# Performance work log

Hardware: AMD Instinct MI355X
Metric: run time of the kernel (lower is better)

Reference implementation:

```python
import jax, jax.numpy as jnp
import numpy as np

NEG_SLOPE = 0.2  # PyG GATConv default leaky_relu slope
NUM_GRAPHS = 64


def gat_layer(x, src, dst, W, a_src, a_dst, b, heads, out_ch, concat, N):
    # x: [N, in_ch] -> h: [N, H, C]
    h = (x @ W).reshape(N, heads, out_ch)
    a_s = jnp.einsum('nhc,hc->nh', h, a_src)  # [N, H]
    a_d = jnp.einsum('nhc,hc->nh', h, a_dst)  # [N, H]
    e = jax.nn.leaky_relu(a_s[src] + a_d[dst], NEG_SLOPE)  # [E, H]
    # segment softmax over edges grouped by destination node
    emax = jax.ops.segment_max(e, dst, num_segments=N)
    emax = jnp.where(jnp.isfinite(emax), emax, 0.0)
    ex = jnp.exp(e - emax[dst])
    denom = jax.ops.segment_sum(ex, dst, num_segments=N)
    alpha = ex / (denom[dst] + 1e-16)  # [E, H]
    out = jax.ops.segment_sum(alpha[:, :, None] * h[src], dst, num_segments=N)  # [N, H, C]
    out = out.reshape(N, heads * out_ch) if concat else out.mean(axis=1)
    return out + b


def setup_inputs() -> dict:
    key = jax.random.key(0)
    ks = jax.random.split(key, 16)
    N, E, F_IN, H, C, NC = 50000, 800000, 128, 4, 64, 200
    x = jax.random.normal(ks[0], (N, F_IN), dtype=jnp.float32)
    edge_index = jax.random.randint(ks[1], (2, E), 0, N, dtype=jnp.int32)
    batch = jnp.sort(jax.random.randint(ks[2], (N,), 0, NUM_GRAPHS, dtype=jnp.int32))
    s = 0.05
    params = dict(
        W1=jax.random.normal(ks[3], (F_IN, H * C), jnp.float32) * s,
        a_src1=jax.random.normal(ks[4], (H, C), jnp.float32) * s,
        a_dst1=jax.random.normal(ks[5], (H, C), jnp.float32) * s,
        b1=jnp.zeros((H * C,), jnp.float32),
        W2=jax.random.normal(ks[6], (H * C, H * C), jnp.float32) * s,
        a_src2=jax.random.normal(ks[7], (H, C), jnp.float32) * s,
        a_dst2=jax.random.normal(ks[8], (H, C), jnp.float32) * s,
        b2=jnp.zeros((H * C,), jnp.float32),
        W3=jax.random.normal(ks[9], (H * C, C), jnp.float32) * s,
        a_src3=jax.random.normal(ks[10], (1, C), jnp.float32) * s,
        a_dst3=jax.random.normal(ks[11], (1, C), jnp.float32) * s,
        b3=jnp.zeros((C,), jnp.float32),
        Wc=jax.random.normal(ks[12], (C, NC), jnp.float32) * s,
        bc=jnp.zeros((NC,), jnp.float32),
    )
    return dict(x=x, edge_index=edge_index, batch=batch, **params)


def reference(x, edge_index, batch,
              W1, a_src1, a_dst1, b1,
              W2, a_src2, a_dst2, b2,
              W3, a_src3, a_dst3, b3,
              Wc, bc):
    N = x.shape[0]
    # PyG GATConv adds self-loops by default
    loop = jnp.arange(N, dtype=edge_index.dtype)
    src = jnp.concatenate([edge_index[0], loop])
    dst = jnp.concatenate([edge_index[1], loop])
    H, C = a_src1.shape
    h = gat_layer(x, src, dst, W1, a_src1, a_dst1, b1, H, C, True, N)
    h = jax.nn.elu(h)  # dropout is identity in eval mode
    h = gat_layer(h, src, dst, W2, a_src2, a_dst2, b2, H, C, True, N)
    h = jax.nn.elu(h)
    h = gat_layer(h, src, dst, W3, a_src3, a_dst3, b3, 1, C, False, N)
    h = jax.nn.elu(h)
    # global mean pool per graph
    sums = jax.ops.segment_sum(h, batch, num_segments=NUM_GRAPHS)
    counts = jax.ops.segment_sum(jnp.ones((N,), h.dtype), batch, num_segments=NUM_GRAPHS)
    pooled = sums / jnp.maximum(counts, 1.0)[:, None]
    return pooled @ Wc + bc
```

## Files before the change

kernel.cpp:

```cpp
#include <hip/hip_runtime.h>


typedef __attribute__((ext_vector_type(8))) __bf16 bf16x8;
typedef __attribute__((ext_vector_type(4))) float f32x4;
typedef __attribute__((ext_vector_type(8))) unsigned short u16x8;

#define LOG2E 1.44269504f

static __device__ __forceinline__ unsigned short f2bf(float f) {
    unsigned u = __float_as_uint(f);
    unsigned r = (u + 0x7fffu + ((u >> 16) & 1u)) >> 16;
    return (unsigned short)r;
}
static __device__ __forceinline__ float bf2f(unsigned short s) {
    return __uint_as_float(((unsigned)s) << 16);
}

static __device__ __forceinline__ void g2lds16(const unsigned short* g,
                                               unsigned short* l) {
    __builtin_amdgcn_global_load_lds(
        (const __attribute__((address_space(1))) unsigned int*)g,
        (__attribute__((address_space(3))) unsigned int*)l, 16, 0, 0);
}

__global__ void count_edges(const int* __restrict__ ei, int* __restrict__ deg,
                            int* __restrict__ epos, int E) {
    int i = blockIdx.x * blockDim.x + threadIdx.x;
    if (i >= E) return;
    int dst = ei[E + i];
    epos[i] = atomicAdd(&deg[dst], 1);
}

__global__ __launch_bounds__(256) void scan_partial(const int* __restrict__ deg,
                                                    int* __restrict__ rowptr,
                                                    int* __restrict__ blockSums, int N) {
    int t = threadIdx.x;
    int lane = t & 63, wv = t >> 6;
    int base = blockIdx.x * 1024 + t * 4;
    int v[4];
#pragma unroll
    for (int j = 0; j < 4; ++j) v[j] = (base + j < N) ? deg[base + j] + 1 : 0;
    int local = v[0] + v[1] + v[2] + v[3];
    int x = local;
#pragma unroll
    for (int off = 1; off < 64; off <<= 1) {
        int y = __shfl_up(x, off);
        if (lane >= off) x += y;
    }
    __shared__ int wsum[4];
    if (lane == 63) wsum[wv] = x;
    __syncthreads();
    int woff = 0;
    for (int i = 0; i < wv; ++i) woff += wsum[i];
    int run = woff + x - local;
#pragma unroll
    for (int j = 0; j < 4; ++j) {
        if (base + j < N) rowptr[base + j] = run;
        run += v[j];
    }
    if (t == 255) blockSums[blockIdx.x] = woff + x;
}

__global__ void scan_blocks(int* __restrict__ blockSums, int* __restrict__ rowptr,
                            int NB, int N) {
    int lane = threadIdx.x;
    int carry = 0;
    for (int b0 = 0; b0 < NB; b0 += 64) {
        int i = b0 + lane;
        int v = (i < NB) ? blockSums[i] : 0;
        int x = v;
#pragma unroll
        for (int off = 1; off < 64; off <<= 1) {
            int y = __shfl_up(x, off);
            if (lane >= off) x += y;
        }
        if (i < NB) blockSums[i] = carry + x - v;
        carry += __shfl(x, 63);
    }
    if (lane == 0) {
        int c = N >> 10;
        int offN;
        if (c < NB) {
            offN = blockSums[c];
        } else {
            blockSums[c] = 0;
            offN = 0;
        }
        rowptr[N] = carry - offN;
    }
}

__global__ void scatter_edges(const int* __restrict__ ei, const int* __restrict__ rowptr,
                              const int* __restrict__ bs,
                              const int* __restrict__ deg, const int* __restrict__ epos,
                              int* __restrict__ srcs, int E, int N) {
    int i = blockIdx.x * blockDim.x + threadIdx.x;
    int tot = E + N;
    if (i >= tot) return;
    if (i < E) {
        int dst = ei[E + i];
        srcs[rowptr[dst] + bs[dst >> 10] + epos[i]] = ei[i];
    } else {
        int d = i - E;
        srcs[rowptr[d] + bs[d >> 10] + deg[d]] = d;
    }
}

__global__ void prep_cast(const float* __restrict__ W1, unsigned short* __restrict__ Wt1,
                          const float* __restrict__ W2, unsigned short* __restrict__ Wt2,
                          const float* __restrict__ W3, unsigned short* __restrict__ Wt3,
                          int n1, int n2, int n3, int F_IN, int HC, int C) {
    int i = blockIdx.x * blockDim.x + threadIdx.x;
    if (i < n1) {
        int n = i / F_IN, k = i - n * F_IN;
        Wt1[i] = f2bf(W1[(size_t)k * HC + n]);
        return;
    }
    i -= n1;
    if (i < n2) {
        int n = i / HC, k = i - n * HC;
        Wt2[i] = f2bf(W2[(size_t)k * HC + n]);
        return;
    }
    i -= n2;
    if (i < n3) {
        int n = i / HC, k = i - n * HC;
        Wt3[i] = f2bf(W3[(size_t)k * C + n]);
    }
}

__global__ void prep_asd(const float* __restrict__ W1, const float* __restrict__ as1,
                         const float* __restrict__ ad1,
                         const float* __restrict__ W2, const float* __restrict__ as2,
                         const float* __restrict__ ad2,
                         const float* __restrict__ W3, const float* __restrict__ as3,
                         const float* __restrict__ ad3,
                         unsigned short* __restrict__ wasd1,
                         unsigned short* __restrict__ wasd2,
                         unsigned short* __restrict__ wasd3) {
    int i = blockIdx.x * blockDim.x + threadIdx.x;
    if (i < 16 * 128) {
        int p = i >> 7, k = i & 127;
        float v = 0.f;
        if (p < 8) {
            const float* a = (p < 4) ? as1 : ad1;
            int hh = p & 3;
            for (int c = 0; c < 64; ++c)
                v += W1[(size_t)k * 256 + hh * 64 + c] * a[hh * 64 + c];
        }
        wasd1[i] = f2bf(v);
        return;
    }
    i -= 16 * 128;
    if (i < 16 * 256) {
        int p = i >> 8, k = i & 255;
        float v = 0.f;
        if (p < 8) {
            const float* a = (p < 4) ? as2 : ad2;
            int hh = p & 3;
            for (int c = 0; c < 64; ++c)
                v += W2[(size_t)k * 256 + hh * 64 + c] * a[hh * 64 + c];
        }
        wasd2[i] = f2bf(v);
        return;
    }
    i -= 16 * 256;
    if (i < 16 * 256) {
        int p = i >> 8, k = i & 255;
        float v = 0.f;
        if (p < 2) {
            const float* a = p ? ad3 : as3;
            for (int c = 0; c < 64; ++c)
                v += W3[(size_t)k * 64 + c] * a[c];
        }
        wasd3[i] = f2bf(v);
    }
}

#define BK 32

template <bool AF32, int WAVES_N>
__global__ __launch_bounds__(256) void gemm_bf16(const void* __restrict__ Av,
                                                 const unsigned short* __restrict__ Bt,
                                                 const unsigned short* __restrict__ Wasd,
                                                 unsigned short* __restrict__ C,
                                                 float* __restrict__ as_o,
                                                 float* __restrict__ ad_o,
                                                 int M, int N, int K, int H) {
    constexpr int BMt = (4 / WAVES_N) * 64;
    constexpr int BNt = WAVES_N * 64;
    constexpr int ASLOTS = BMt * 4;
    constexpr int ROUNDS = (BMt + BNt) / 64;
    constexpr bool ASD_ALL = (WAVES_N == 1);
    __shared__ unsigned short As[2][BMt * BK];
    __shared__ unsigned short Bs[2][BNt * BK];
    __shared__ unsigned short Ws[2][16 * BK];
    int t = threadIdx.x;
    int bm = blockIdx.y * BMt;
    int wave = t >> 6, lane = t & 63;
    int wm = (wave / WAVES_N) * 64, wn = (wave % WAVES_N) * 64;
    int quad = lane >> 4, mr = lane & 15;

    f32x4 zero = {0.f, 0.f, 0.f, 0.f};
    f32x4 acc[4][4];
#pragma unroll
    for (int i = 0; i < 4; ++i)
#pragma unroll
        for (int j = 0; j < 4; ++j) acc[i][j] = zero;
    f32x4 acc4[4];
#pragma unroll
    for (int i = 0; i < 4; ++i) acc4[i] = zero;

    int sw = quad ^ ((mr >> 1) & 3);
    int aoff[4], boff[4];
#pragma unroll
    for (int i = 0; i < 4; ++i) {
        aoff[i] = (wm + i * 16 + mr) * BK + sw * 8;
        boff[i] = (wn + i * 16 + mr) * BK + sw * 8;
    }

    auto stage_ab = [&](int bsel, int kk) {
        const unsigned short* Ab = (const unsigned short*)Av;
#pragma unroll
        for (int r = 0; r < ROUNDS; ++r) {
            int slotw = r * 256 + wave * 64;
            int slot = slotw + lane;
            if (slotw < ASLOTS) {
                int row = slot >> 2;
                int sg = (slot & 3) ^ ((row >> 1) & 3);
                int gra = bm + row;
                if (gra < M)
                    g2lds16(&Ab[(size_t)gra * K + kk + sg * 8], &As[bsel][slotw * 8]);
            } else {
                int bslot = slot - ASLOTS;
                int row = bslot >> 2;
                int sg = (bslot & 3) ^ ((row >> 1) & 3);
                g2lds16(&Bt[(size_t)row * K + kk + sg * 8], &Bs[bsel][(slotw - ASLOTS) * 8]);
            }
        }
        if (wave == 0)
            g2lds16(&Wasd[(size_t)(lane >> 2) * K + kk + (lane & 3) * 8], &Ws[bsel][0]);
    };
    auto stage_b_af32 = [&](int bsel, int kk) {
#pragma unroll
        for (int r = 0; r < BNt / 64; ++r) {
            int slotw = r * 256 + wave * 64;
            int bslot = slotw + lane;
            int row = bslot >> 2;
            int sg = (bslot & 3) ^ ((row >> 1) & 3);
            g2lds16(&Bt[(size_t)row * K + kk + sg * 8], &Bs[bsel][slotw * 8]);
        }
        if (wave == 0)
            g2lds16(&Wasd[(size_t)(lane >> 2) * K + kk + (lane & 3) * 8], &Ws[bsel][0]);
    };
    auto loadA_f32 = [&](int kk, float4& lo, float4& hi) {
        int slot = t, row = slot >> 2;
        int sg = (slot & 3) ^ ((row >> 1) & 3);
        int gra = bm + row;
        lo = make_float4(0.f, 0.f, 0.f, 0.f); hi = lo;
        if (gra < M) {
            const float* Af = (const float*)Av;
            lo = *(const float4*)&Af[(size_t)gra * K + kk + sg * 8];
            hi = *(const float4*)&Af[(size_t)gra * K + kk + sg * 8 + 4];
        }
    };
    auto writeA = [&](int bsel, float4 lo, float4 hi) {
        int slot = t;
        *(ushort4*)&As[bsel][slot * 8]     = make_ushort4(f2bf(lo.x), f2bf(lo.y), f2bf(lo.z), f2bf(lo.w));
        *(ushort4*)&As[bsel][slot * 8 + 4] = make_ushort4(f2bf(hi.x), f2bf(hi.y), f2bf(hi.z), f2bf(hi.w));
    };

    const int nt = K / BK;
    int cur = 0;

    if (AF32) {
        float4 l0, h0;
        loadA_f32(0, l0, h0);
        writeA(0, l0, h0);
        stage_b_af32(0, 0);
    } else {
        stage_ab(0, 0);
    }
    __syncthreads();

    for (int ts = 0; ts < nt; ++ts) {
        int nxt = cur ^ 1;
        bool more = (ts + 1 < nt);
        float4 plo, phi;
        if (more) {
            if (AF32) {
                loadA_f32((ts + 1) * BK, plo, phi);
                stage_b_af32(nxt, (ts + 1) * BK);
            } else {
                stage_ab(nxt, (ts + 1) * BK);
            }
        }
        bf16x8 af[4], bfr[4];
#pragma unroll
        for (int i = 0; i < 4; ++i) {
            af[i]  = *(bf16x8*)&As[cur][aoff[i]];
            bfr[i] = *(bf16x8*)&Bs[cur][boff[i]];
        }
#pragma unroll
        for (int i = 0; i < 4; ++i)
#pragma unroll
            for (int j = 0; j < 4; ++j)
                acc[i][j] = __builtin_amdgcn_mfma_f32_16x16x32_bf16(af[i], bfr[j], acc[i][j], 0, 0, 0);
        if (ASD_ALL || wave == 0) {
            bf16x8 wsf = *(bf16x8*)&Ws[cur][mr * BK + quad * 8];
#pragma unroll
            for (int i = 0; i < 4; ++i)
                acc4[i] = __builtin_amdgcn_mfma_f32_16x16x32_bf16(af[i], wsf, acc4[i], 0, 0, 0);
        }
        if (more && AF32) writeA(nxt, plo, phi);
        __syncthreads();
        cur = nxt;
    }

    if ((ASD_ALL || wave == 0) && mr < 2 * H) {
#pragma unroll
        for (int i = 0; i < 4; ++i)
#pragma unroll
            for (int r = 0; r < 4; ++r) {
                int grow = bm + wm + i * 16 + quad * 4 + r;
                if (grow >= M) continue;
                float v = acc4[i][r] * LOG2E;
                if (mr < H) as_o[(size_t)grow * H + mr] = v;
                else        ad_o[(size_t)grow * H + (mr - H)] = v;
            }
    }

#pragma unroll
    for (int i = 0; i < 4; ++i) {
#pragma unroll
        for (int r = 0; r < 4; ++r) {
            int grow = bm + wm + i * 16 + quad * 4 + r;
            if (grow >= M) continue;
#pragma unroll
            for (int j = 0; j < 4; ++j) {
                int gcol = wn + j * 16 + mr;
                C[(size_t)grow * N + gcol] = f2bf(acc[i][j][r]);
            }
        }
    }
}

template <int H, int NPW, int VPL, bool OUTF32>
__global__ __launch_bounds__(256) void gat_aggregate(const unsigned short* __restrict__ hbuf,
                                                     const float* __restrict__ as_i,
                                                     const float* __restrict__ ad_i,
                                                     const int* __restrict__ rowptr,
                                                     const int* __restrict__ bs,
                                                     const int* __restrict__ srcs,
                                                     const float* __restrict__ bias,
                                                     void* __restrict__ out_v, int N) {
    constexpr int LPN = 64 / NPW;
    constexpr int HC = LPN * VPL;
    int wid = (blockIdx.x * blockDim.x + threadIdx.x) >> 6;
    int lane = threadIdx.x & 63;
    int sub = lane / LPN;
    int li  = lane % LPN;
    int node = wid * NPW + sub;
    if (node >= N) return;
    int row = rowptr[node] + bs[node >> 10];
    int end = rowptr[node + 1] + bs[(node + 1) >> 10];
    int len = end - row;
    const int hd_lane = (li * VPL) >> 6;

    float advh = ad_i[(size_t)node * H + hd_lane];

    float acc[VPL];
#pragma unroll
    for (int j = 0; j < VPL; ++j) acc[j] = 0.f;
    float l = 0.f;

    const int U = 8;
    for (int base = 0; base < len; base += U) {
        int s[U];
        float cf[U];
#pragma unroll
        for (int u = 0; u < U; ++u) {
            int idx = base + u;
            int ii = row + ((idx < len) ? idx : (len - 1));
            s[u] = srcs[ii];
        }
#pragma unroll
        for (int u = 0; u < U; ++u) cf[u] = as_i[(size_t)s[u] * H + hd_lane];
        if (VPL == 8) {
            u16x8 r[U];
#pragma unroll
            for (int u = 0; u < U; ++u)
                r[u] = *(const u16x8*)&hbuf[(size_t)s[u] * HC + li * 8];
#pragma unroll
            for (int u = 0; u < U; ++u) {
                float e = cf[u] + advh;
                e = fmaxf(e, 0.2f * e);
                float wgt = (base + u < len) ? exp2f(e) : 0.f;
                l += wgt;
#pragma unroll
                for (int j = 0; j < 8; ++j) acc[j] += wgt * bf2f(r[u][j]);
            }
        } else {
            ushort4 r[U];
#pragma unroll
            for (int u = 0; u < U; ++u)
                r[u] = *(const ushort4*)&hbuf[(size_t)s[u] * HC + li * 4];
#pragma unroll
            for (int u = 0; u < U; ++u) {
                float e = cf[u] + advh;
                e = fmaxf(e, 0.2f * e);
                float wgt = (base + u < len) ? exp2f(e) : 0.f;
                l += wgt;
                acc[0] += wgt * bf2f(r[u].x);
                acc[1] += wgt * bf2f(r[u].y);
                acc[2] += wgt * bf2f(r[u].z);
                acc[3] += wgt * bf2f(r[u].w);
            }
        }
    }

    float inv_l = 1.f / (l + 1e-16f);
    float vals[VPL];
#pragma unroll
    for (int j = 0; j < VPL; ++j) {
        float v = acc[j] * inv_l + bias[li * VPL + j];
        vals[j] = (v > 0.f) ? v : (__expf(v) - 1.f);
    }
    if (OUTF32) {
        float* out = (float*)out_v;
        if (VPL == 4) {
            float4 o = make_float4(vals[0], vals[1], vals[2], vals[3]);
            *(float4*)&out[(size_t)node * HC + li * 4] = o;
        } else {
#pragma unroll
            for (int j = 0; j < VPL; ++j)
                out[(size_t)node * HC + li * VPL + j] = vals[j];
        }
    } else {
        unsigned short* out = (unsigned short*)out_v;
        if (VPL == 8) {
            u16x8 o;
#pragma unroll
            for (int j = 0; j < 8; ++j) o[j] = f2bf(vals[j]);
            *(u16x8*)&out[(size_t)node * HC + li * 8] = o;
        } else {
            ushort4 o;
            o.x = f2bf(vals[0]); o.y = f2bf(vals[1]);
            o.z = f2bf(vals[2]); o.w = f2bf(vals[3]);
            *(ushort4*)&out[(size_t)node * HC + li * 4] = o;
        }
    }
}

#define POOL_CHUNK 128
__global__ __launch_bounds__(256) void pool_kernel(const float* __restrict__ hf,
                                                   const int* __restrict__ batch,
                                                   float* __restrict__ sums,
                                                   float* __restrict__ counts, int N) {
    int t = threadIdx.x;
    int c = t & 63, sub = t >> 6;
    int start = blockIdx.x * POOL_CHUNK;
    int end = min(start + POOL_CHUNK, N);
    float acc = 0.f, cnt = 0.f;
    int cur = -1;
    for (int n = start + sub; n < end; n += 4) {
        int g = batch[n];
        if (g != cur) {
            if (cur >= 0) {
                atomicAdd(&sums[cur * 64 + c], acc);
                if (c == 0) atomicAdd(&counts[cur], cnt);
            }
            cur = g; acc = 0.f; cnt = 0.f;
        }
        acc += hf[(size_t)n * 64 + c];
        cnt += 1.f;
    }
    if (cur >= 0) {
        atomicAdd(&sums[cur * 64 + c], acc);
        if (c == 0) atomicAdd(&counts[cur], cnt);
    }
}

__global__ void classify(const float* __restrict__ sums, const float* __restrict__ counts,
                         const float* __restrict__ Wc, const float* __restrict__ bc,
                         float* __restrict__ out, int NC) {
    __shared__ float p[64];
    int g = blockIdx.x;
    if (threadIdx.x < 64) {
        float cnt = fmaxf(counts[g], 1.0f);
        p[threadIdx.x] = sums[g * 64 + threadIdx.x] / cnt;
    }
    __syncthreads();
    int k = threadIdx.x;
    if (k < NC) {
        float acc = bc[k];
        for (int c = 0; c < 64; ++c) acc += p[c] * Wc[c * NC + k];
        out[g * NC + k] = acc;
    }
}

static inline size_t align_up(size_t x, size_t a) { return (x + a - 1) / a * a; }

extern "C" void kernel_launch(void* const* d_in, const int* in_sizes, int n_in,
                              void* d_out, int out_size, void* d_ws, size_t ws_size,
                              hipStream_t stream) {
    const float* x      = (const float*)d_in[0];
    const int*   ei     = (const int*)d_in[1];
    const int*   batch  = (const int*)d_in[2];
    const float* W1     = (const float*)d_in[3];
    const float* a_src1 = (const float*)d_in[4];
    const float* a_dst1 = (const float*)d_in[5];
    const float* b1     = (const float*)d_in[6];
    const float* W2     = (const float*)d_in[7];
    const float* a_src2 = (const float*)d_in[8];
    const float* a_dst2 = (const float*)d_in[9];
    const float* b2     = (const float*)d_in[10];
    const float* W3     = (const float*)d_in[11];
    const float* a_src3 = (const float*)d_in[12];
    const float* a_dst3 = (const float*)d_in[13];
    const float* b3     = (const float*)d_in[14];
    const float* Wc     = (const float*)d_in[15];
    const float* bc     = (const float*)d_in[16];

    const int N    = in_sizes[2];
    const int E    = in_sizes[1] / 2;
    const int F_IN = in_sizes[0] / N;
    const int HC   = in_sizes[6];
    const int C    = in_sizes[14];
    const int NC   = in_sizes[16];
    const int Etot = E + N;
    const int NB   = (N + 1023) / 1024;
    const int NPB  = (N + POOL_CHUNK - 1) / POOL_CHUNK;

    char* w = (char*)d_ws;
    size_t off = 0;
    auto alloc = [&](size_t bytes) -> void* {
        void* p = w + off;
        off = align_up(off + bytes, 256);
        return p;
    };
    int*   deg    = (int*)alloc((size_t)N * 4);
    float* sums   = (float*)alloc((size_t)(64 * 64 + 64) * 4);
    float* counts = sums + 64 * 64;
    int*   rowptr = (int*)alloc((size_t)(N + 1) * 4);
    int*   epos   = (int*)alloc((size_t)E * 4);
    int*   srcs   = (int*)alloc((size_t)Etot * 4);
    int*   bsums  = (int*)alloc((size_t)(NB + 1) * 4);
    float* as_buf = (float*)alloc((size_t)N * 4 * 4);
    float* ad_buf = (float*)alloc((size_t)N * 4 * 4);
    unsigned short* Wt1 = (unsigned short*)alloc((size_t)HC * F_IN * 2);
    unsigned short* Wt2 = (unsigned short*)alloc((size_t)HC * HC * 2);
    unsigned short* Wt3 = (unsigned short*)alloc((size_t)C * HC * 2);
    unsigned short* wasd1 = (unsigned short*)alloc((size_t)16 * F_IN * 2);
    unsigned short* wasd2 = (unsigned short*)alloc((size_t)16 * HC * 2);
    unsigned short* wasd3 = (unsigned short*)alloc((size_t)16 * HC * 2);
    unsigned short* hA  = (unsigned short*)alloc((size_t)N * HC * 2);
    unsigned short* hB  = (unsigned short*)alloc((size_t)N * HC * 2);
    unsigned short* hC  = (unsigned short*)alloc((size_t)N * C * 2);
    float* bufF   = (float*)alloc((size_t)N * C * 4);

    const int TPB = 256;

    hipMemsetAsync(deg, 0, (char*)(sums + 64 * 64 + 64) - (char*)deg, stream);

    count_edges<<<(E + TPB - 1) / TPB, TPB, 0, stream>>>(ei, deg, epos, E);
    scan_partial<<<NB, 256, 0, stream>>>(deg, rowptr, bsums, N);
    scan_blocks<<<1, 64, 0, stream>>>(bsums, rowptr, NB, N);
    scatter_edges<<<(Etot + TPB - 1) / TPB, TPB, 0, stream>>>(ei, rowptr, bsums, deg, epos, srcs, E, N);

    int n1 = HC * F_IN, n2 = HC * HC, n3 = C * HC;
    int ntot = n1 + n2 + n3;
    prep_cast<<<(ntot + TPB - 1) / TPB, TPB, 0, stream>>>(
        W1, Wt1, W2, Wt2, W3, Wt3, n1, n2, n3, F_IN, HC, C);
    int nasd = 16 * F_IN + 16 * HC + 16 * HC;
    prep_asd<<<(nasd + TPB - 1) / TPB, TPB, 0, stream>>>(
        W1, a_src1, a_dst1, W2, a_src2, a_dst2, W3, a_src3, a_dst3,
        wasd1, wasd2, wasd3);

    dim3 gWide(1, (N + 63) / 64);
    dim3 gNarrow(1, (N + 255) / 256);
    int aggBlocks12 = (((N + 1) / 2) + 3) / 4;
    int aggBlocks3  = (((N + 3) / 4) + 3) / 4;

    gemm_bf16<true, 4><<<gWide, 256, 0, stream>>>(x, Wt1, wasd1, hA, as_buf, ad_buf, N, HC, F_IN, 4);
    gat_aggregate<4, 2, 8, false><<<aggBlocks12, 256, 0, stream>>>(hA, as_buf, ad_buf, rowptr, bsums, srcs, b1, hB, N);

    gemm_bf16<false, 4><<<gWide, 256, 0, stream>>>(hB, Wt2, wasd2, hA, as_buf, ad_buf, N, HC, HC, 4);
    gat_aggregate<4, 2, 8, false><<<aggBlocks12, 256, 0, stream>>>(hA, as_buf, ad_buf, rowptr, bsums, srcs, b2, hB, N);

    gemm_bf16<false, 1><<<gNarrow, 256, 0, stream>>>(hB, Wt3, wasd3, hC, as_buf, ad_buf, N, C, HC, 1);
    gat_aggregate<1, 4, 4, true><<<aggBlocks3, 256, 0, stream>>>(hC, as_buf, ad_buf, rowptr, bsums, srcs, b3, bufF, N);

    pool_kernel<<<NPB, 256, 0, stream>>>(bufF, batch, sums, counts, N);
    classify<<<64, 256, 0, stream>>>(sums, counts, Wc, bc, (float*)d_out, NC);
}
```

Before: 398.6 us.

## Merge weight prep kernels, drop GEMM double buffering, split aggregation launches

The two weight-preparation kernels become one launch. The GEMM loses its double-buffered LDS pipeline and uses single-buffered staging with two barriers per K step, halving shared memory and possibly raising occupancy, but it no longer overlaps loads with MFMA work. The layer 1 and 2 aggregations are each split into two launches over node halves. This adds launch overhead and brings no obvious benefit on a single stream.

```diff
diff --git a/kernel.cpp b/kernel.cpp
--- a/kernel.cpp
+++ b/kernel.cpp
@@ -106,10 +106,16 @@
     }
 }
 
-__global__ void prep_cast(const float* __restrict__ W1, unsigned short* __restrict__ Wt1,
-                          const float* __restrict__ W2, unsigned short* __restrict__ Wt2,
-                          const float* __restrict__ W3, unsigned short* __restrict__ Wt3,
-                          int n1, int n2, int n3, int F_IN, int HC, int C) {
+__global__ void prep_weights(const float* __restrict__ W1, unsigned short* __restrict__ Wt1,
+                             const float* __restrict__ W2, unsigned short* __restrict__ Wt2,
+                             const float* __restrict__ W3, unsigned short* __restrict__ Wt3,
+                             const float* __restrict__ as1, const float* __restrict__ ad1,
+                             const float* __restrict__ as2, const float* __restrict__ ad2,
+                             const float* __restrict__ as3, const float* __restrict__ ad3,
+                             unsigned short* __restrict__ wasd1,
+                             unsigned short* __restrict__ wasd2,
+                             unsigned short* __restrict__ wasd3,
+                             int n1, int n2, int n3, int F_IN, int HC, int C) {
     int i = blockIdx.x * blockDim.x + threadIdx.x;
     if (i < n1) {
         int n = i / F_IN, k = i - n * F_IN;
@@ -126,19 +132,9 @@
     if (i < n3) {
         int n = i / HC, k = i - n * HC;
         Wt3[i] = f2bf(W3[(size_t)k * C + n]);
-    }
-}
-
-__global__ void prep_asd(const float* __restrict__ W1, const float* __restrict__ as1,
-                         const float* __restrict__ ad1,
-                         const float* __restrict__ W2, const float* __restrict__ as2,
-                         const float* __restrict__ ad2,
-                         const float* __restrict__ W3, const float* __restrict__ as3,
-                         const float* __restrict__ ad3,
-                         unsigned short* __restrict__ wasd1,
-                         unsigned short* __restrict__ wasd2,
-                         unsigned short* __restrict__ wasd3) {
-    int i = blockIdx.x * blockDim.x + threadIdx.x;
+        return;
+    }
+    i -= n3;
     if (i < 16 * 128) {
         int p = i >> 7, k = i & 127;
         float v = 0.f;
@@ -192,9 +188,9 @@
     constexpr int ASLOTS = BMt * 4;
     constexpr int ROUNDS = (BMt + BNt) / 64;
     constexpr bool ASD_ALL = (WAVES_N == 1);
-    __shared__ unsigned short As[2][BMt * BK];
-    __shared__ unsigned short Bs[2][BNt * BK];
-    __shared__ unsigned short Ws[2][16 * BK];
+    __shared__ unsigned short As[BMt * BK];
+    __shared__ unsigned short Bs[BNt * BK];
+    __shared__ unsigned short Ws[16 * BK];
     int t = threadIdx.x;
     int bm = blockIdx.y * BMt;
     int wave = t >> 6, lane = t & 63;
@@ -219,87 +215,64 @@
         boff[i] = (wn + i * 16 + mr) * BK + sw * 8;
     }
 
-    auto stage_ab = [&](int bsel, int kk) {
-        const unsigned short* Ab = (const unsigned short*)Av;
-#pragma unroll
-        for (int r = 0; r < ROUNDS; ++r) {
-            int slotw = r * 256 + wave * 64;
-            int slot = slotw + lane;
-            if (slotw < ASLOTS) {
-                int row = slot >> 2;
-                int sg = (slot & 3) ^ ((row >> 1) & 3);
-                int gra = bm + row;
-                if (gra < M)
-                    g2lds16(&Ab[(size_t)gra * K + kk + sg * 8], &As[bsel][slotw * 8]);
-            } else {
-                int bslot = slot - ASLOTS;
+    for (int k0 = 0; k0 < K; k0 += BK) {
+        ushort4 ua0, ua1;
+        if (AF32) {
+            int slot = t;
+            int row = slot >> 2;
+            int sg = (slot & 3) ^ ((row >> 1) & 3);
+            int gra = bm + row;
+            float4 lo = make_float4(0.f, 0.f, 0.f, 0.f), hi = lo;
+            if (gra < M) {
+                const float* Af = (const float*)Av;
+                lo = *(const float4*)&Af[(size_t)gra * K + k0 + sg * 8];
+                hi = *(const float4*)&Af[(size_t)gra * K + k0 + sg * 8 + 4];
+            }
+            ua0 = make_ushort4(f2bf(lo.x), f2bf(lo.y), f2bf(lo.z), f2bf(lo.w));
+            ua1 = make_ushort4(f2bf(hi.x), f2bf(hi.y), f2bf(hi.z), f2bf(hi.w));
+        }
+        __syncthreads();
+        if (AF32) {
+            int slot = t;
+            *(ushort4*)&As[slot * 8]     = ua0;
+            *(ushort4*)&As[slot * 8 + 4] = ua1;
+#pragma unroll
+            for (int r = 0; r < BNt / 64; ++r) {
+                int slotw = r * 256 + wave * 64;
+                int bslot = slotw + lane;
                 int row = bslot >> 2;
                 int sg = (bslot & 3) ^ ((row >> 1) & 3);
-                g2lds16(&Bt[(size_t)row * K + kk + sg * 8], &Bs[bsel][(slotw - ASLOTS) * 8]);
+                g2lds16(&Bt[(size_t)row * K + k0 + sg * 8], &Bs[slotw * 8]);
+            }
+        } else {
+            const unsigned short* Ab = (const unsigned short*)Av;
+#pragma unroll
+            for (int r = 0; r < ROUNDS; ++r) {
+                int slotw = r * 256 + wave * 64;
+                int slot = slotw + lane;
+                if (slotw < ASLOTS) {
+                    int row = slot >> 2;
+                    int sg = (slot & 3) ^ ((row >> 1) & 3);
+                    int gra = bm + row;
+                    if (gra < M)
+                        g2lds16(&Ab[(size_t)gra * K + k0 + sg * 8], &As[slotw * 8]);
+                } else {
+                    int bslot = slot - ASLOTS;
+                    int row = bslot >> 2;
+                    int sg = (bslot & 3) ^ ((row >> 1) & 3);
+                    g2lds16(&Bt[(size_t)row * K + k0 + sg * 8], &Bs[(slotw - ASLOTS) * 8]);
+                }
             }
         }
         if (wave == 0)
-            g2lds16(&Wasd[(size_t)(lane >> 2) * K + kk + (lane & 3) * 8], &Ws[bsel][0]);
-    };
-    auto stage_b_af32 = [&](int bsel, int kk) {
-#pragma unroll
-        for (int r = 0; r < BNt / 64; ++r) {
-            int slotw = r * 256 + wave * 64;
-            int bslot = slotw + lane;
-            int row = bslot >> 2;
-            int sg = (bslot & 3) ^ ((row >> 1) & 3);
-            g2lds16(&Bt[(size_t)row * K + kk + sg * 8], &Bs[bsel][slotw * 8]);
-        }
-        if (wave == 0)
-            g2lds16(&Wasd[(size_t)(lane >> 2) * K + kk + (lane & 3) * 8], &Ws[bsel][0]);
-    };
-    auto loadA_f32 = [&](int kk, float4& lo, float4& hi) {
-        int slot = t, row = slot >> 2;
-        int sg = (slot & 3) ^ ((row >> 1) & 3);
-        int gra = bm + row;
-        lo = make_float4(0.f, 0.f, 0.f, 0.f); hi = lo;
-        if (gra < M) {
-            const float* Af = (const float*)Av;
-            lo = *(const float4*)&Af[(size_t)gra * K + kk + sg * 8];
-            hi = *(const float4*)&Af[(size_t)gra * K + kk + sg * 8 + 4];
-        }
-    };
-    auto writeA = [&](int bsel, float4 lo, float4 hi) {
-        int slot = t;
-        *(ushort4*)&As[bsel][slot * 8]     = make_ushort4(f2bf(lo.x), f2bf(lo.y), f2bf(lo.z), f2bf(lo.w));
-        *(ushort4*)&As[bsel][slot * 8 + 4] = make_ushort4(f2bf(hi.x), f2bf(hi.y), f2bf(hi.z), f2bf(hi.w));
-    };
-
-    const int nt = K / BK;
-    int cur = 0;
-
-    if (AF32) {
-        float4 l0, h0;
-        loadA_f32(0, l0, h0);
-        writeA(0, l0, h0);
-        stage_b_af32(0, 0);
-    } else {
-        stage_ab(0, 0);
-    }
-    __syncthreads();
-
-    for (int ts = 0; ts < nt; ++ts) {
-        int nxt = cur ^ 1;
-        bool more = (ts + 1 < nt);
-        float4 plo, phi;
-        if (more) {
-            if (AF32) {
-                loadA_f32((ts + 1) * BK, plo, phi);
-                stage_b_af32(nxt, (ts + 1) * BK);
-            } else {
-                stage_ab(nxt, (ts + 1) * BK);
-            }
-        }
+            g2lds16(&Wasd[(size_t)(lane >> 2) * K + k0 + (lane & 3) * 8], &Ws[0]);
+        __syncthreads();
+
         bf16x8 af[4], bfr[4];
 #pragma unroll
         for (int i = 0; i < 4; ++i) {
-            af[i]  = *(bf16x8*)&As[cur][aoff[i]];
-            bfr[i] = *(bf16x8*)&Bs[cur][boff[i]];
+            af[i]  = *(bf16x8*)&As[aoff[i]];
+            bfr[i] = *(bf16x8*)&Bs[boff[i]];
         }
 #pragma unroll
         for (int i = 0; i < 4; ++i)
@@ -307,14 +280,11 @@
             for (int j = 0; j < 4; ++j)
                 acc[i][j] = __builtin_amdgcn_mfma_f32_16x16x32_bf16(af[i], bfr[j], acc[i][j], 0, 0, 0);
         if (ASD_ALL || wave == 0) {
-            bf16x8 wsf = *(bf16x8*)&Ws[cur][mr * BK + quad * 8];
+            bf16x8 wsf = *(bf16x8*)&Ws[mr * BK + quad * 8];
 #pragma unroll
             for (int i = 0; i < 4; ++i)
                 acc4[i] = __builtin_amdgcn_mfma_f32_16x16x32_bf16(af[i], wsf, acc4[i], 0, 0, 0);
         }
-        if (more && AF32) writeA(nxt, plo, phi);
-        __syncthreads();
-        cur = nxt;
     }
 
     if ((ASD_ALL || wave == 0) && mr < 2 * H) {
@@ -353,15 +323,16 @@
                                                      const int* __restrict__ bs,
                                                      const int* __restrict__ srcs,
                                                      const float* __restrict__ bias,
-                                                     void* __restrict__ out_v, int N) {
+                                                     void* __restrict__ out_v,
+                                                     int n0, int nend) {
     constexpr int LPN = 64 / NPW;
     constexpr int HC = LPN * VPL;
     int wid = (blockIdx.x * blockDim.x + threadIdx.x) >> 6;
     int lane = threadIdx.x & 63;
     int sub = lane / LPN;
     int li  = lane % LPN;
-    int node = wid * NPW + sub;
-    if (node >= N) return;
+    int node = n0 + wid * NPW + sub;
+    if (node >= nend) return;
     int row = rowptr[node] + bs[node >> 10];
     int end = rowptr[node + 1] + bs[(node + 1) >> 10];
     int len = end - row;
@@ -569,27 +540,31 @@
     scatter_edges<<<(Etot + TPB - 1) / TPB, TPB, 0, stream>>>(ei, rowptr, bsums, deg, epos, srcs, E, N);
 
     int n1 = HC * F_IN, n2 = HC * HC, n3 = C * HC;
-    int ntot = n1 + n2 + n3;
-    prep_cast<<<(ntot + TPB - 1) / TPB, TPB, 0, stream>>>(
-        W1, Wt1, W2, Wt2, W3, Wt3, n1, n2, n3, F_IN, HC, C);
-    int nasd = 16 * F_IN + 16 * HC + 16 * HC;
-    prep_asd<<<(nasd + TPB - 1) / TPB, TPB, 0, stream>>>(
-        W1, a_src1, a_dst1, W2, a_src2, a_dst2, W3, a_src3, a_dst3,
-        wasd1, wasd2, wasd3);
+    int ntot = n1 + n2 + n3 + 16 * F_IN + 16 * HC + 16 * HC;
+    prep_weights<<<(ntot + TPB - 1) / TPB, TPB, 0, stream>>>(
+        W1, Wt1, W2, Wt2, W3, Wt3,
+        a_src1, a_dst1, a_src2, a_dst2, a_src3, a_dst3,
+        wasd1, wasd2, wasd3, n1, n2, n3, F_IN, HC, C);
 
     dim3 gWide(1, (N + 63) / 64);
     dim3 gNarrow(1, (N + 255) / 256);
-    int aggBlocks12 = (((N + 1) / 2) + 3) / 4;
-    int aggBlocks3  = (((N + 3) / 4) + 3) / 4;
+
+    int nh = ((N / 2) + 7) / 8 * 8;
+    if (nh > N) nh = N;
+    int gAgg1 = (nh + 7) / 8;
+    int gAgg2 = (N - nh + 7) / 8;
+    int aggBlocks3 = (((N + 3) / 4) + 3) / 4;
 
     gemm_bf16<true, 4><<<gWide, 256, 0, stream>>>(x, Wt1, wasd1, hA, as_buf, ad_buf, N, HC, F_IN, 4);
-    gat_aggregate<4, 2, 8, false><<<aggBlocks12, 256, 0, stream>>>(hA, as_buf, ad_buf, rowptr, bsums, srcs, b1, hB, N);
+    gat_aggregate<4, 2, 8, false><<<gAgg1, 256, 0, stream>>>(hA, as_buf, ad_buf, rowptr, bsums, srcs, b1, hB, 0, nh);
+    gat_aggregate<4, 2, 8, false><<<gAgg2, 256, 0, stream>>>(hA, as_buf, ad_buf, rowptr, bsums, srcs, b1, hB, nh, N);
 
     gemm_bf16<false, 4><<<gWide, 256, 0, stream>>>(hB, Wt2, wasd2, hA, as_buf, ad_buf, N, HC, HC, 4);
-    gat_aggregate<4, 2, 8, false><<<aggBlocks12, 256, 0, stream>>>(hA, as_buf, ad_buf, rowptr, bsums, srcs, b2, hB, N);
+    gat_aggregate<4, 2, 8, false><<<gAgg1, 256, 0, stream>>>(hA, as_buf, ad_buf, rowptr, bsums, srcs, b2, hB, 0, nh);
+    gat_aggregate<4, 2, 8, false><<<gAgg2, 256, 0, stream>>>(hA, as_buf, ad_buf, rowptr, bsums, srcs, b2, hB, nh, N);
 
     gemm_bf16<false, 1><<<gNarrow, 256, 0, stream>>>(hB, Wt3, wasd3, hC, as_buf, ad_buf, N, C, HC, 1);
-    gat_aggregate<1, 4, 4, true><<<aggBlocks3, 256, 0, stream>>>(hC, as_buf, ad_buf, rowptr, bsums, srcs, b3, bufF, N);
+    gat_aggregate<1, 4, 4, true><<<aggBlocks3, 256, 0, stream>>>(hC, as_buf, ad_buf, rowptr, bsums, srcs, b3, bufF, 0, N);
 
     pool_kernel<<<NPB, 256, 0, stream>>>(bufF, batch, sums, counts, N);
     classify<<<64, 256, 0, stream>>>(sums, counts, Wc, bc, (float*)d_out, NC);
```

Result: slower. 414.7 us (+4.1%).
